# Kernel tuning notes

Hardware: AMD Instinct MI355X
Metric: run time of the kernel (lower is better)

## Reference

```python
import jax, jax.numpy as jnp
import numpy as np

EXPERT_NUM = 8
SEQ_LEN = 2048
FREQ_LEN = SEQ_LEN // 2 + 1
B, C = 32, 512


def setup_inputs() -> dict:
    key = jax.random.key(0)
    k1, k2, k3 = jax.random.split(key, 3)
    x = jax.random.normal(k1, (B, C, SEQ_LEN), dtype=jnp.float32)
    band_boundaries = jax.random.uniform(k2, (EXPERT_NUM - 1,), dtype=jnp.float32)
    gate_w = jax.random.normal(k3, (EXPERT_NUM, FREQ_LEN), dtype=jnp.float32) / np.sqrt(FREQ_LEN)
    gate_b = jnp.zeros((EXPERT_NUM,), dtype=jnp.float32)
    return {"x": x, "band_boundaries": band_boundaries, "gate_w": gate_w, "gate_b": gate_b}


def reference(x, band_boundaries, gate_w, gate_b):
    # x: [B, C, L].  Normalize across channels per (batch, time) position.
    xp = jnp.transpose(x, (0, 2, 1))                       # [B, L, C]
    x_mean = jnp.mean(xp, axis=2, keepdims=True)           # [B, L, 1]
    xc = xp - x_mean
    x_var = jnp.var(xc, axis=2, keepdims=True, ddof=1) + 1e-5  # unbiased, as torch.var
    xn = xc / jnp.sqrt(x_var)
    x_norm = jnp.transpose(xn, (0, 2, 1))                  # [B, C, L]

    freq_x = jnp.fft.rfft(x_norm, axis=-1)                 # [B, C, F] complex
    F = FREQ_LEN

    # Learnable band boundaries -> integer bin boundaries per expert.
    b = jnp.sort(jax.nn.sigmoid(band_boundaries))
    b = jnp.concatenate([jnp.zeros((1,), b.dtype), b, jnp.ones((1,), b.dtype)])
    idx = (b * F).astype(jnp.int32)
    idx = idx.at[-1].set(F)                                # [E+1]

    # Per-frequency-bin expert membership: [E, F] 0/1 mask.
    f = jnp.arange(F)
    member = ((f[None, :] >= idx[:-1, None]) & (f[None, :] < idx[1:, None])).astype(x.dtype)

    # Gating over mean spectral magnitude.
    gating_input = jnp.abs(freq_x).mean(axis=1)            # [B, F]
    gating_scores = jax.nn.softmax(gating_input @ gate_w.T + gate_b, axis=-1)  # [B, E]

    # Fused: per-bin gate weight = sum_e g[b,e] * member[e,f] (no E copies of freq_x).
    w = gating_scores @ member                             # [B, F]
    combined_freq = freq_x * w[:, None, :].astype(freq_x.dtype)

    combined = jnp.fft.irfft(combined_freq, n=SEQ_LEN, axis=-1)  # [B, C, L]

    # De-normalize.
    cp = jnp.transpose(combined, (0, 2, 1))                # [B, L, C]
    out = cp * jnp.sqrt(x_var) + x_mean
    return jnp.transpose(out, (0, 2, 1))                   # [B, C, L]
```

## Files before the change

### kernel.cpp

```cpp
#include <hip/hip_runtime.h>
#include <math.h>

#define NB 32
#define NC 512
#define NF 1025

#define WS_MEAN 0
#define WS_SSTD 65536
#define WS_RSTD 131072
#define WS_GACC 196608
#define WS_WGT  229408
#define WS_PART 262208
#define WS_END_SPLIT (262208 + 262144)
#define WS_SPEC WS_END_SPLIT
#define WS_SPEC_FLOATS (NB * NC * 2048)
#define WS_END_CACHE (WS_SPEC + WS_SPEC_FLOATS)

#define PIDX(a) ((a) + ((a) >> 4))

__device__ __forceinline__ void stage4(const float* __restrict__ sr,
                                       const float* __restrict__ si,
                                       float* __restrict__ dr,
                                       float* __restrict__ di,
                                       const int ls, const float w1c, const float w1s,
                                       const bool fwd) {
  const int t = threadIdx.x;
  const int s = 1 << ls;
  const int q = t & (s - 1);
  const int p = t >> ls;
  __syncthreads();
  const float ar = sr[PIDX(t)],       ai = si[PIDX(t)];
  const float br = sr[PIDX(t + 256)], bi = si[PIDX(t + 256)];
  const float cr = sr[PIDX(t + 512)], ci = si[PIDX(t + 512)];
  const float er = sr[PIDX(t + 768)], ei = si[PIDX(t + 768)];
  const float apcr = ar + cr, apci = ai + ci;
  const float amcr = ar - cr, amci = ai - ci;
  const float bpdr = br + er, bpdi = bi + ei;
  const float bmdr = br - er, bmdi = bi - ei;
  const float w2r = w1c * w1c - w1s * w1s, w2i = 2.0f * w1c * w1s;
  const float w3r = w2r * w1c - w2i * w1s, w3i = w2r * w1s + w2i * w1c;
  float u1r, u1i, u3r, u3i;
  if (fwd) {
    u1r = amcr + bmdi; u1i = amci - bmdr;
    u3r = amcr - bmdi; u3i = amci + bmdr;
  } else {
    u1r = amcr - bmdi; u1i = amci + bmdr;
    u3r = amcr + bmdi; u3i = amci - bmdr;
  }
  const float x0r = apcr + bpdr, x0i = apci + bpdi;
  const float v2r = apcr - bpdr, v2i = apci - bpdi;
  const float x1r = w1c * u1r - w1s * u1i, x1i = w1c * u1i + w1s * u1r;
  const float x2r = w2r * v2r - w2i * v2i, x2i = w2r * v2i + w2i * v2r;
  const float x3r = w3r * u3r - w3i * u3i, x3i = w3r * u3i + w3i * u3r;
  const int base = q + ((p << 2) << ls);
  dr[PIDX(base)] = x0r;             di[PIDX(base)] = x0i;
  dr[PIDX(base + s)] = x1r;         di[PIDX(base + s)] = x1i;
  dr[PIDX(base + 2 * s)] = x2r;     di[PIDX(base + 2 * s)] = x2i;
  dr[PIDX(base + 3 * s)] = x3r;     di[PIDX(base + 3 * s)] = x3i;
}

__device__ __forceinline__ void stage4_nt(const float* __restrict__ sr,
                                          const float* __restrict__ si,
                                          float* __restrict__ dr,
                                          float* __restrict__ di,
                                          const bool fwd) {
  const int t = threadIdx.x;
  __syncthreads();
  const float ar = sr[PIDX(t)],       ai = si[PIDX(t)];
  const float br = sr[PIDX(t + 256)], bi = si[PIDX(t + 256)];
  const float cr = sr[PIDX(t + 512)], ci = si[PIDX(t + 512)];
  const float er = sr[PIDX(t + 768)], ei = si[PIDX(t + 768)];
  const float apcr = ar + cr, apci = ai + ci;
  const float amcr = ar - cr, amci = ai - ci;
  const float bpdr = br + er, bpdi = bi + ei;
  const float bmdr = br - er, bmdi = bi - ei;
  float u1r, u1i, u3r, u3i;
  if (fwd) {
    u1r = amcr + bmdi; u1i = amci - bmdr;
    u3r = amcr - bmdi; u3i = amci + bmdr;
  } else {
    u1r = amcr - bmdi; u1i = amci + bmdr;
    u3r = amcr + bmdi; u3i = amci - bmdr;
  }
  dr[PIDX(t)] = apcr + bpdr;        di[PIDX(t)] = apci + bpdi;
  dr[PIDX(t + 256)] = u1r;          di[PIDX(t + 256)] = u1i;
  dr[PIDX(t + 512)] = apcr - bpdr;  di[PIDX(t + 512)] = apci - bpdi;
  dr[PIDX(t + 768)] = u3r;          di[PIDX(t + 768)] = u3i;
}

__device__ __forceinline__ void fft_twiddles(int t, float& c0, float& s0,
                                             float& c1, float& s1,
                                             float& c2, float& s2,
                                             float& c3, float& s3) {
  __sincosf(-0.00613592315f * (float)t, &s0, &c0);
  __sincosf(-0.02454369261f * (float)(t >> 2), &s1, &c1);
  __sincosf(-0.09817477042f * (float)(t >> 4), &s2, &c2);
  __sincosf(-0.39269908170f * (float)(t >> 6), &s3, &c3);
}

__device__ __forceinline__ void fft_fwd1024(float* Ar, float* Ai, float* Br, float* Bi,
                                            float c0, float s0, float c1, float s1,
                                            float c2, float s2, float c3, float s3) {
  stage4(Ar, Ai, Br, Bi, 0, c0, s0, true);
  stage4(Br, Bi, Ar, Ai, 2, c1, s1, true);
  stage4(Ar, Ai, Br, Bi, 4, c2, s2, true);
  stage4(Br, Bi, Ar, Ai, 6, c3, s3, true);
  stage4_nt(Ar, Ai, Br, Bi, true);
}
__device__ __forceinline__ void fft_inv1024(float* Ar, float* Ai, float* Br, float* Bi,
                                            float c0, float s0, float c1, float s1,
                                            float c2, float s2, float c3, float s3) {
  stage4(Br, Bi, Ar, Ai, 0, c0, -s0, false);
  stage4(Ar, Ai, Br, Bi, 2, c1, -s1, false);
  stage4(Br, Bi, Ar, Ai, 4, c2, -s2, false);
  stage4(Ar, Ai, Br, Bi, 6, c3, -s3, false);
  stage4_nt(Br, Bi, Ar, Ai, false);
}

__global__ __launch_bounds__(256) void kmoments(const float* __restrict__ x,
                                                float* __restrict__ ws) {
  const int b = blockIdx.x >> 3;
  const int l = ((blockIdx.x & 7) << 8) + threadIdx.x;
  const float* px = x + (size_t)b * (NC * 2048) + l;
  float sum = 0.f, sq = 0.f;
#pragma unroll 16
  for (int c = 0; c < NC; ++c) {
    float v = px[(size_t)c * 2048];
    sum += v;
    sq = fmaf(v, v, sq);
  }
  float mean = sum * (1.0f / 512.0f);
  float var = fmaf(-512.0f * mean, mean, sq) * (1.0f / 511.0f) + 1e-5f;
  float ss = sqrtf(var);
  int o = (b << 11) + l;
  ws[WS_MEAN + o] = mean;
  ws[WS_SSTD + o] = ss;
  ws[WS_RSTD + o] = 1.0f / ss;
}

__global__ __launch_bounds__(256) void kmoments_part(const float* __restrict__ x,
                                                     float* __restrict__ ws) {
  const int b = blockIdx.x >> 3;
  const int l = ((blockIdx.x & 7) << 8) + threadIdx.x;
  const int half = blockIdx.y;
  const float* px = x + (size_t)b * (NC * 2048) + (size_t)(half * 256) * 2048 + l;
  float sum = 0.f, sq = 0.f;
#pragma unroll 16
  for (int c = 0; c < 256; ++c) {
    float v = px[(size_t)c * 2048];
    sum += v;
    sq = fmaf(v, v, sq);
  }
  int o = (b << 11) + l;
  float2* part = (float2*)(ws + WS_PART) + (half << 16) + o;
  float2 pv; pv.x = sum; pv.y = sq;
  *part = pv;
}

__global__ __launch_bounds__(256) void kmoments_fin(float* __restrict__ ws) {
  const int o = blockIdx.x * 256 + threadIdx.x;
  const float2* part = (const float2*)(ws + WS_PART);
  float2 p0 = part[o];
  float2 p1 = part[(1 << 16) + o];
  float sum = p0.x + p1.x, sq = p0.y + p1.y;
  float mean = sum * (1.0f / 512.0f);
  float var = fmaf(-512.0f * mean, mean, sq) * (1.0f / 511.0f) + 1e-5f;
  float ss = sqrtf(var);
  ws[WS_MEAN + o] = mean;
  ws[WS_SSTD + o] = ss;
  ws[WS_RSTD + o] = 1.0f / ss;
}

__global__ __launch_bounds__(256) void kspec(const float* __restrict__ x,
                                             float* __restrict__ ws,
                                             float2* __restrict__ zout) {
  __shared__ float Ar[1088], Ai[1088], Br[1088], Bi[1088];
  const int tid = threadIdx.x;
  const int b = blockIdx.x >> 6;
  const int c0 = (blockIdx.x & 63) << 3;
  const float2* mean2 = (const float2*)(ws + WS_MEAN) + ((size_t)b << 10);
  const float2* rstd2 = (const float2*)(ws + WS_RSTD) + ((size_t)b << 10);
  float2 mv[4], rv[4];
#pragma unroll
  for (int j = 0; j < 4; ++j) {
    mv[j] = mean2[tid + (j << 8)];
    rv[j] = rstd2[tid + (j << 8)];
  }
  float w1s, w1c, w2s, w2c;
  __sincosf(-0.00306796158f * (float)tid, &w1s, &w1c);
  __sincosf(-0.00306796158f * (float)(tid + 256), &w2s, &w2c);
  float c0t, s0t, c1t, s1t, c2t, s2t, c3t, s3t;
  fft_twiddles(tid, c0t, s0t, c1t, s1t, c2t, s2t, c3t, s3t);
  float acc0 = 0.f, acc1 = 0.f, acc2 = 0.f, acc3 = 0.f, acc4 = 0.f;
  const float2* xrow = (const float2*)x + ((size_t)(b * NC + c0) << 10);
  float2 v[4];
#pragma unroll
  for (int j = 0; j < 4; ++j) v[j] = xrow[tid + (j << 8)];
  for (int r = 0; r < 8; ++r) {
#pragma unroll
    for (int j = 0; j < 4; ++j) {
      const int n = tid + (j << 8);
      Ar[PIDX(n)] = (v[j].x - mv[j].x) * rv[j].x;
      Ai[PIDX(n)] = (v[j].y - mv[j].y) * rv[j].y;
    }
    if (r < 7) {
      const float2* nx = xrow + ((size_t)(r + 1) << 10);
#pragma unroll
      for (int j = 0; j < 4; ++j) v[j] = nx[tid + (j << 8)];
    }
    fft_fwd1024(Ar, Ai, Br, Bi, c0t, s0t, c1t, s1t, c2t, s2t, c3t, s3t);
    __syncthreads();
    if (zout) {
      float2* zrow = zout + ((size_t)(b * NC + c0 + r) << 10);
#pragma unroll
      for (int j = 0; j < 4; ++j) {
        const int n = tid + (j << 8);
        float2 zv; zv.x = Br[PIDX(n)]; zv.y = Bi[PIDX(n)];
        zrow[n] = zv;
      }
    }
    if (tid == 0) {
      float zr = Br[PIDX(0)], zi = Bi[PIDX(0)];
      acc0 += fabsf(zr + zi);
      acc1 += fabsf(zr - zi);
      float mr = Br[PIDX(512)], mi = Bi[PIDX(512)];
      acc4 += sqrtf(mr * mr + mi * mi);
    } else {
      const int k = tid;
      float zkr = Br[PIDX(k)], zki = Bi[PIDX(k)];
      float zmr = Br[PIDX(1024 - k)], zmi = Bi[PIDX(1024 - k)];
      float Ar_ = 0.5f * (zkr + zmr), Ai_ = 0.5f * (zki - zmi);
      float Br_ = 0.5f * (zki + zmi), Bi_ = -0.5f * (zkr - zmr);
      float WBr = Br_ * w1c - Bi_ * w1s, WBi = Br_ * w1s + Bi_ * w1c;
      float Xr = Ar_ + WBr, Xi = Ai_ + WBi;
      float Yr = Ar_ - WBr, Yi = Ai_ - WBi;
      acc0 += sqrtf(Xr * Xr + Xi * Xi);
      acc1 += sqrtf(Yr * Yr + Yi * Yi);
    }
    {
      const int k = tid + 256;
      float zkr = Br[PIDX(k)], zki = Bi[PIDX(k)];
      float zmr = Br[PIDX(1024 - k)], zmi = Bi[PIDX(1024 - k)];
      float Ar_ = 0.5f * (zkr + zmr), Ai_ = 0.5f * (zki - zmi);
      float Br_ = 0.5f * (zki + zmi), Bi_ = -0.5f * (zkr - zmr);
      float WBr = Br_ * w2c - Bi_ * w2s, WBi = Br_ * w2s + Bi_ * w2c;
      float Xr = Ar_ + WBr, Xi = Ai_ + WBi;
      float Yr = Ar_ - WBr, Yi = Ai_ - WBi;
      acc2 += sqrtf(Xr * Xr + Xi * Xi);
      acc3 += sqrtf(Yr * Yr + Yi * Yi);
    }
  }
  float* g = ws + WS_GACC + b * NF;
  atomicAdd(g + tid, acc0);
  atomicAdd(g + 1024 - tid, acc1);
  atomicAdd(g + tid + 256, acc2);
  atomicAdd(g + 768 - tid, acc3);
  if (tid == 0) atomicAdd(g + 512, acc4);
}

__global__ __launch_bounds__(256) void kgate(float* __restrict__ ws,
                                             const float* __restrict__ gw,
                                             const float* __restrict__ gb,
                                             const float* __restrict__ bb) {
  const float* gacc = ws + WS_GACC;
  float* wgt = ws + WS_WGT;
  const int b = blockIdx.x;
  const int tid = threadIdx.x;
  __shared__ float red[256];
  __shared__ float sc[8];
  __shared__ int sidx[9];
  float acc[8];
#pragma unroll
  for (int e = 0; e < 8; ++e) acc[e] = 0.f;
  for (int f = tid; f < NF; f += 256) {
    float g = gacc[b * NF + f] * (1.0f / 512.0f);
#pragma unroll
    for (int e = 0; e < 8; ++e) acc[e] = fmaf(g, gw[e * NF + f], acc[e]);
  }
#pragma unroll
  for (int e = 0; e < 8; ++e) {
    __syncthreads();
    red[tid] = acc[e];
    __syncthreads();
    for (int s2 = 128; s2 > 0; s2 >>= 1) {
      if (tid < s2) red[tid] += red[tid + s2];
      __syncthreads();
    }
    if (tid == 0) sc[e] = red[0] + gb[e];
  }
  __syncthreads();
  if (tid == 0) {
    float mx = sc[0];
    for (int e = 1; e < 8; ++e) mx = fmaxf(mx, sc[e]);
    float sum = 0.f;
    float ex[8];
    for (int e = 0; e < 8; ++e) { ex[e] = expf(sc[e] - mx); sum += ex[e]; }
    for (int e = 0; e < 8; ++e) sc[e] = ex[e] / sum;
    float sv[7];
    for (int i2 = 0; i2 < 7; ++i2) sv[i2] = 1.0f / (1.0f + expf(-bb[i2]));
    for (int i2 = 1; i2 < 7; ++i2) {
      float key = sv[i2];
      int j2 = i2 - 1;
      while (j2 >= 0 && sv[j2] > key) { sv[j2 + 1] = sv[j2]; --j2; }
      sv[j2 + 1] = key;
    }
    sidx[0] = 0;
    for (int i2 = 0; i2 < 7; ++i2) sidx[i2 + 1] = (int)(sv[i2] * 1025.0f);
    sidx[8] = 1025;
  }
  __syncthreads();
  for (int f = tid; f < NF; f += 256) {
    float wv = 0.f;
#pragma unroll
    for (int e = 0; e < 8; ++e)
      if (f >= sidx[e] && f < sidx[e + 1]) wv += sc[e];
    wgt[b * NF + f] = wv;
  }
}

__device__ __forceinline__ void combine_pair(float* __restrict__ zr_, float* __restrict__ zi_,
                                             int k, float wc, float ws_, float wk, float wmk) {
  const int ik = PIDX(k), im = PIDX(1024 - k);
  float zkr = zr_[ik], zki = zi_[ik];
  float zmr = zr_[im], zmi = zi_[im];
  float Ar_ = 0.5f * (zkr + zmr), Ai_ = 0.5f * (zki - zmi);
  float Br2 = 0.5f * (zki + zmi), Bi2 = -0.5f * (zkr - zmr);
  float WBr = Br2 * wc - Bi2 * ws_, WBi = Br2 * ws_ + Bi2 * wc;
  float Xr = Ar_ + WBr, Xi = Ai_ + WBi;
  float Xcr = Ar_ - WBr, Xci = Ai_ - WBi;
  float XpR = wk * Xr, XpI = wk * Xi;
  float XcpR = wmk * Xcr, XcpI = wmk * Xci;
  float Apr = 0.5f * (XpR + XcpR), Api = 0.5f * (XpI + XcpI);
  float Er = 0.5f * (XpR - XcpR), Ei = 0.5f * (XpI - XcpI);
  float Bpr = Er * wc + Ei * ws_;
  float Bpi = Ei * wc - Er * ws_;
  zr_[ik] = Apr - Bpi;  zi_[ik] = Api + Bpr;
  zr_[im] = Apr + Bpi;  zi_[im] = Bpr - Api;
}

__global__ __launch_bounds__(256) void kapply(const float* __restrict__ x,
                                              float* __restrict__ out,
                                              const float* __restrict__ ws) {
  __shared__ float Ar[1088], Ai[1088], Br[1088], Bi[1088];
  const int tid = threadIdx.x;
  const int b = blockIdx.x >> 9;
  const float2* mean2 = (const float2*)(ws + WS_MEAN) + ((size_t)b << 10);
  const float2* sstd2 = (const float2*)(ws + WS_SSTD) + ((size_t)b << 10);
  const float2* rstd2 = (const float2*)(ws + WS_RSTD) + ((size_t)b << 10);
  const float2* x2 = (const float2*)x + ((size_t)blockIdx.x << 10);
  const float* wrow = ws + WS_WGT + b * NF;
  float wk1 = wrow[tid];
  float wm1 = wrow[1024 - tid];
  float wk2 = wrow[tid + 256];
  float wm2 = wrow[768 - tid];
  float wmid = wrow[512];
  float w1s, w1c, w2s, w2c;
  __sincosf(-0.00306796158f * (float)tid, &w1s, &w1c);
  __sincosf(-0.00306796158f * (float)(tid + 256), &w2s, &w2c);
  float c0t, s0t, c1t, s1t, c2t, s2t, c3t, s3t;
  fft_twiddles(tid, c0t, s0t, c1t, s1t, c2t, s2t, c3t, s3t);
  float2 mv[4], rv[4];
#pragma unroll
  for (int j = 0; j < 4; ++j) {
    mv[j] = mean2[tid + (j << 8)];
    rv[j] = rstd2[tid + (j << 8)];
  }
#pragma unroll
  for (int j = 0; j < 4; ++j) {
    const int n = tid + (j << 8);
    float2 v = x2[n];
    Ar[PIDX(n)] = (v.x - mv[j].x) * rv[j].x;
    Ai[PIDX(n)] = (v.y - mv[j].y) * rv[j].y;
  }
  fft_fwd1024(Ar, Ai, Br, Bi, c0t, s0t, c1t, s1t, c2t, s2t, c3t, s3t);
  __syncthreads();
  if (tid == 0) {
    float zr = Br[PIDX(0)], zi = Bi[PIDX(0)];
    float X0 = (zr + zi) * wk1;
    float XM = (zr - zi) * wm1;
    Br[PIDX(0)] = 0.5f * (X0 + XM);
    Bi[PIDX(0)] = 0.5f * (X0 - XM);
    Br[PIDX(512)] *= wmid;
    Bi[PIDX(512)] *= wmid;
  } else {
    combine_pair(Br, Bi, tid, w1c, w1s, wk1, wm1);
  }
  combine_pair(Br, Bi, tid + 256, w2c, w2s, wk2, wm2);
  fft_inv1024(Ar, Ai, Br, Bi, c0t, s0t, c1t, s1t, c2t, s2t, c3t, s3t);
  const float inv = 1.0f / 1024.0f;
  float2* out2 = (float2*)out + ((size_t)blockIdx.x << 10);
#pragma unroll
  for (int j = 0; j < 4; ++j) {
    const int n = tid + (j << 8);
    float2 ss = sstd2[n];
    float2 o;
    o.x = fmaf(Ar[PIDX(n)] * inv, ss.x, mv[j].x);
    o.y = fmaf(Ai[PIDX(n)] * inv, ss.y, mv[j].y);
    out2[n] = o;
  }
}

__global__ __launch_bounds__(256) void kapply_z(const float2* __restrict__ z,
                                                float* __restrict__ out,
                                                const float* __restrict__ ws) {
  __shared__ float Ar[1088], Ai[1088], Br[1088], Bi[1088];
  const int tid = threadIdx.x;
  const int b = blockIdx.x >> 9;
  const float2* mean2 = (const float2*)(ws + WS_MEAN) + ((size_t)b << 10);
  const float2* sstd2 = (const float2*)(ws + WS_SSTD) + ((size_t)b << 10);
  const float* wrow = ws + WS_WGT + b * NF;
  float wk1 = wrow[tid];
  float wm1 = wrow[1024 - tid];
  float wk2 = wrow[tid + 256];
  float wm2 = wrow[768 - tid];
  float wmid = wrow[512];
  float w1s, w1c, w2s, w2c;
  __sincosf(-0.00306796158f * (float)tid, &w1s, &w1c);
  __sincosf(-0.00306796158f * (float)(tid + 256), &w2s, &w2c);
  float c0t, s0t, c1t, s1t, c2t, s2t, c3t, s3t;
  fft_twiddles(tid, c0t, s0t, c1t, s1t, c2t, s2t, c3t, s3t);
  const float2* zrow = z + ((size_t)blockIdx.x << 10);
  float2 mv[4], ssv[4];
#pragma unroll
  for (int j = 0; j < 4; ++j) {
    mv[j] = mean2[tid + (j << 8)];
    ssv[j] = sstd2[tid + (j << 8)];
  }
#pragma unroll
  for (int j = 0; j < 4; ++j) {
    const int n = tid + (j << 8);
    float2 v = zrow[n];
    Br[PIDX(n)] = v.x;
    Bi[PIDX(n)] = v.y;
  }
  __syncthreads();
  if (tid == 0) {
    float zr = Br[PIDX(0)], zi = Bi[PIDX(0)];
    float X0 = (zr + zi) * wk1;
    float XM = (zr - zi) * wm1;
    Br[PIDX(0)] = 0.5f * (X0 + XM);
    Bi[PIDX(0)] = 0.5f * (X0 - XM);
    Br[PIDX(512)] *= wmid;
    Bi[PIDX(512)] *= wmid;
  } else {
    combine_pair(Br, Bi, tid, w1c, w1s, wk1, wm1);
  }
  combine_pair(Br, Bi, tid + 256, w2c, w2s, wk2, wm2);
  fft_inv1024(Ar, Ai, Br, Bi, c0t, s0t, c1t, s1t, c2t, s2t, c3t, s3t);
  const float inv = 1.0f / 1024.0f;
  float2* out2 = (float2*)out + ((size_t)blockIdx.x << 10);
#pragma unroll
  for (int j = 0; j < 4; ++j) {
    const int n = tid + (j << 8);
    float2 o;
    o.x = fmaf(Ar[PIDX(n)] * inv, ssv[j].x, mv[j].x);
    o.y = fmaf(Ai[PIDX(n)] * inv, ssv[j].y, mv[j].y);
    out2[n] = o;
  }
}

extern "C" void kernel_launch(void* const* d_in, const int* in_sizes, int n_in,
                              void* d_out, int out_size, void* d_ws, size_t ws_size,
                              hipStream_t stream) {
  const float* x = (const float*)d_in[0];
  const float* bb = (const float*)d_in[1];
  const float* gw = (const float*)d_in[2];
  const float* gb = (const float*)d_in[3];
  float* ws = (float*)d_ws;
  float* out = (float*)d_out;

  const bool split = ws_size >= (size_t)WS_END_SPLIT * sizeof(float);
  const bool cache = ws_size >= (size_t)WS_END_CACHE * sizeof(float);

  hipMemsetAsync((char*)d_ws + WS_GACC * sizeof(float), 0, (NB * NF) * sizeof(float), stream);
  if (split) {
    kmoments_part<<<dim3(NB * 8, 2), dim3(256), 0, stream>>>(x, ws);
    kmoments_fin<<<dim3(256), dim3(256), 0, stream>>>(ws);
  } else {
    kmoments<<<dim3(NB * 8), dim3(256), 0, stream>>>(x, ws);
  }
  kspec<<<dim3(NB * 64), dim3(256), 0, stream>>>(x, ws,
      cache ? (float2*)(ws + WS_SPEC) : nullptr);
  kgate<<<dim3(NB), dim3(256), 0, stream>>>(ws, gw, gb, bb);
  if (cache) {
    kapply_z<<<dim3(NB * NC), dim3(256), 0, stream>>>((const float2*)(ws + WS_SPEC), out, ws);
  } else {
    kapply<<<dim3(NB * NC), dim3(256), 0, stream>>>(x, out, ws);
  }
}
```

Measured before the change: 350.4 us.

## Keep first and last FFT stages in registers and replace gating atomics with partials

The first radix-4 FFT stage now reads its inputs directly from registers instead of staging them through shared memory. The final stage returns its results in registers, which feed the global writes and the output denormalisation directly, saving LDS round trips and one barrier per FFT. Gating magnitude sums are now written as per-block partials to an extra workspace region and reduced in kgate. This removes the atomics and the memset, but makes kgate read 64 rows per batch element.

```diff
diff --git a/kernel.cpp b/kernel.cpp
--- a/kernel.cpp
+++ b/kernel.cpp
@@ -15,6 +15,9 @@
 #define WS_SPEC WS_END_SPLIT
 #define WS_SPEC_FLOATS (NB * NC * 2048)
 #define WS_END_CACHE (WS_SPEC + WS_SPEC_FLOATS)
+#define WS_GPART WS_END_CACHE
+#define WS_GPART_FLOATS (NB * 64 * NF)
+#define WS_END_GPART (WS_GPART + WS_GPART_FLOATS)
 
 #define PIDX(a) ((a) + ((a) >> 4))
 
@@ -59,11 +62,42 @@
   dr[PIDX(base + 3 * s)] = x3r;     di[PIDX(base + 3 * s)] = x3i;
 }
 
-__device__ __forceinline__ void stage4_nt(const float* __restrict__ sr,
-                                          const float* __restrict__ si,
-                                          float* __restrict__ dr,
-                                          float* __restrict__ di,
-                                          const bool fwd) {
+__device__ __forceinline__ void stage0_reg(const float2 z0, const float2 z1,
+                                           const float2 z2, const float2 z3,
+                                           float* __restrict__ dr, float* __restrict__ di,
+                                           const float w1c, const float w1s,
+                                           const bool fwd) {
+  const int t = threadIdx.x;
+  const float apcr = z0.x + z2.x, apci = z0.y + z2.y;
+  const float amcr = z0.x - z2.x, amci = z0.y - z2.y;
+  const float bpdr = z1.x + z3.x, bpdi = z1.y + z3.y;
+  const float bmdr = z1.x - z3.x, bmdi = z1.y - z3.y;
+  const float w2r = w1c * w1c - w1s * w1s, w2i = 2.0f * w1c * w1s;
+  const float w3r = w2r * w1c - w2i * w1s, w3i = w2r * w1s + w2i * w1c;
+  float u1r, u1i, u3r, u3i;
+  if (fwd) {
+    u1r = amcr + bmdi; u1i = amci - bmdr;
+    u3r = amcr - bmdi; u3i = amci + bmdr;
+  } else {
+    u1r = amcr - bmdi; u1i = amci + bmdr;
+    u3r = amcr + bmdi; u3i = amci - bmdr;
+  }
+  const float x0r = apcr + bpdr, x0i = apci + bpdi;
+  const float v2r = apcr - bpdr, v2i = apci - bpdi;
+  const float x1r = w1c * u1r - w1s * u1i, x1i = w1c * u1i + w1s * u1r;
+  const float x2r = w2r * v2r - w2i * v2i, x2i = w2r * v2i + w2i * v2r;
+  const float x3r = w3r * u3r - w3i * u3i, x3i = w3r * u3i + w3i * u3r;
+  const int base = t << 2;
+  dr[PIDX(base)] = x0r;         di[PIDX(base)] = x0i;
+  dr[PIDX(base + 1)] = x1r;     di[PIDX(base + 1)] = x1i;
+  dr[PIDX(base + 2)] = x2r;     di[PIDX(base + 2)] = x2i;
+  dr[PIDX(base + 3)] = x3r;     di[PIDX(base + 3)] = x3i;
+}
+
+__device__ __forceinline__ void stage_nt_reg(const float* __restrict__ sr,
+                                             const float* __restrict__ si,
+                                             float2& o0, float2& o1, float2& o2, float2& o3,
+                                             const bool fwd) {
   const int t = threadIdx.x;
   __syncthreads();
   const float ar = sr[PIDX(t)],       ai = si[PIDX(t)];
@@ -82,10 +116,10 @@
     u1r = amcr - bmdi; u1i = amci + bmdr;
     u3r = amcr + bmdi; u3i = amci - bmdr;
   }
-  dr[PIDX(t)] = apcr + bpdr;        di[PIDX(t)] = apci + bpdi;
-  dr[PIDX(t + 256)] = u1r;          di[PIDX(t + 256)] = u1i;
-  dr[PIDX(t + 512)] = apcr - bpdr;  di[PIDX(t + 512)] = apci - bpdi;
-  dr[PIDX(t + 768)] = u3r;          di[PIDX(t + 768)] = u3i;
+  o0.x = apcr + bpdr;  o0.y = apci + bpdi;
+  o1.x = u1r;          o1.y = u1i;
+  o2.x = apcr - bpdr;  o2.y = apci - bpdi;
+  o3.x = u3r;          o3.y = u3i;
 }
 
 __device__ __forceinline__ void fft_twiddles(int t, float& c0, float& s0,
@@ -96,25 +130,6 @@
   __sincosf(-0.02454369261f * (float)(t >> 2), &s1, &c1);
   __sincosf(-0.09817477042f * (float)(t >> 4), &s2, &c2);
   __sincosf(-0.39269908170f * (float)(t >> 6), &s3, &c3);
-}
-
-__device__ __forceinline__ void fft_fwd1024(float* Ar, float* Ai, float* Br, float* Bi,
-                                            float c0, float s0, float c1, float s1,
-                                            float c2, float s2, float c3, float s3) {
-  stage4(Ar, Ai, Br, Bi, 0, c0, s0, true);
-  stage4(Br, Bi, Ar, Ai, 2, c1, s1, true);
-  stage4(Ar, Ai, Br, Bi, 4, c2, s2, true);
-  stage4(Br, Bi, Ar, Ai, 6, c3, s3, true);
-  stage4_nt(Ar, Ai, Br, Bi, true);
-}
-__device__ __forceinline__ void fft_inv1024(float* Ar, float* Ai, float* Br, float* Bi,
-                                            float c0, float s0, float c1, float s1,
-                                            float c2, float s2, float c3, float s3) {
-  stage4(Br, Bi, Ar, Ai, 0, c0, -s0, false);
-  stage4(Ar, Ai, Br, Bi, 2, c1, -s1, false);
-  stage4(Br, Bi, Ar, Ai, 4, c2, -s2, false);
-  stage4(Ar, Ai, Br, Bi, 6, c3, -s3, false);
-  stage4_nt(Br, Bi, Ar, Ai, false);
 }
 
 __global__ __launch_bounds__(256) void kmoments(const float* __restrict__ x,
@@ -173,7 +188,8 @@
 
 __global__ __launch_bounds__(256) void kspec(const float* __restrict__ x,
                                              float* __restrict__ ws,
-                                             float2* __restrict__ zout) {
+                                             float2* __restrict__ zout,
+                                             float* __restrict__ gpart) {
   __shared__ float Ar[1088], Ai[1088], Br[1088], Bi[1088];
   const int tid = threadIdx.x;
   const int b = blockIdx.x >> 6;
@@ -197,27 +213,35 @@
 #pragma unroll
   for (int j = 0; j < 4; ++j) v[j] = xrow[tid + (j << 8)];
   for (int r = 0; r < 8; ++r) {
+    float2 zz[4];
 #pragma unroll
     for (int j = 0; j < 4; ++j) {
-      const int n = tid + (j << 8);
-      Ar[PIDX(n)] = (v[j].x - mv[j].x) * rv[j].x;
-      Ai[PIDX(n)] = (v[j].y - mv[j].y) * rv[j].y;
+      zz[j].x = (v[j].x - mv[j].x) * rv[j].x;
+      zz[j].y = (v[j].y - mv[j].y) * rv[j].y;
     }
     if (r < 7) {
       const float2* nx = xrow + ((size_t)(r + 1) << 10);
 #pragma unroll
       for (int j = 0; j < 4; ++j) v[j] = nx[tid + (j << 8)];
     }
-    fft_fwd1024(Ar, Ai, Br, Bi, c0t, s0t, c1t, s1t, c2t, s2t, c3t, s3t);
+    __syncthreads();
+    stage0_reg(zz[0], zz[1], zz[2], zz[3], Br, Bi, c0t, s0t, true);
+    stage4(Br, Bi, Ar, Ai, 2, c1t, s1t, true);
+    stage4(Ar, Ai, Br, Bi, 4, c2t, s2t, true);
+    stage4(Br, Bi, Ar, Ai, 6, c3t, s3t, true);
+    float2 o0, o1, o2, o3;
+    stage_nt_reg(Ar, Ai, o0, o1, o2, o3, true);
+    Br[PIDX(tid)] = o0.x;        Bi[PIDX(tid)] = o0.y;
+    Br[PIDX(tid + 256)] = o1.x;  Bi[PIDX(tid + 256)] = o1.y;
+    Br[PIDX(tid + 512)] = o2.x;  Bi[PIDX(tid + 512)] = o2.y;
+    Br[PIDX(tid + 768)] = o3.x;  Bi[PIDX(tid + 768)] = o3.y;
     __syncthreads();
     if (zout) {
       float2* zrow = zout + ((size_t)(b * NC + c0 + r) << 10);
-#pragma unroll
-      for (int j = 0; j < 4; ++j) {
-        const int n = tid + (j << 8);
-        float2 zv; zv.x = Br[PIDX(n)]; zv.y = Bi[PIDX(n)];
-        zrow[n] = zv;
-      }
+      zrow[tid] = o0;
+      zrow[tid + 256] = o1;
+      zrow[tid + 512] = o2;
+      zrow[tid + 768] = o3;
     }
     if (tid == 0) {
       float zr = Br[PIDX(0)], zi = Bi[PIDX(0)];
@@ -250,18 +274,28 @@
       acc3 += sqrtf(Yr * Yr + Yi * Yi);
     }
   }
-  float* g = ws + WS_GACC + b * NF;
-  atomicAdd(g + tid, acc0);
-  atomicAdd(g + 1024 - tid, acc1);
-  atomicAdd(g + tid + 256, acc2);
-  atomicAdd(g + 768 - tid, acc3);
-  if (tid == 0) atomicAdd(g + 512, acc4);
+  if (gpart) {
+    float* prow = gpart + (size_t)blockIdx.x * NF;
+    prow[tid] = acc0;
+    prow[1024 - tid] = acc1;
+    prow[tid + 256] = acc2;
+    prow[768 - tid] = acc3;
+    if (tid == 0) prow[512] = acc4;
+  } else {
+    float* g = ws + WS_GACC + b * NF;
+    atomicAdd(g + tid, acc0);
+    atomicAdd(g + 1024 - tid, acc1);
+    atomicAdd(g + tid + 256, acc2);
+    atomicAdd(g + 768 - tid, acc3);
+    if (tid == 0) atomicAdd(g + 512, acc4);
+  }
 }
 
 __global__ __launch_bounds__(256) void kgate(float* __restrict__ ws,
                                              const float* __restrict__ gw,
                                              const float* __restrict__ gb,
-                                             const float* __restrict__ bb) {
+                                             const float* __restrict__ bb,
+                                             const float* __restrict__ gpart) {
   const float* gacc = ws + WS_GACC;
   float* wgt = ws + WS_WGT;
   const int b = blockIdx.x;
@@ -273,7 +307,16 @@
 #pragma unroll
   for (int e = 0; e < 8; ++e) acc[e] = 0.f;
   for (int f = tid; f < NF; f += 256) {
-    float g = gacc[b * NF + f] * (1.0f / 512.0f);
+    float g;
+    if (gpart) {
+      const float* gp = gpart + (size_t)b * 64 * NF + f;
+      g = 0.f;
+#pragma unroll 8
+      for (int j = 0; j < 64; ++j) g += gp[j * NF];
+    } else {
+      g = gacc[b * NF + f];
+    }
+    g *= (1.0f / 512.0f);
 #pragma unroll
     for (int e = 0; e < 8; ++e) acc[e] = fmaf(g, gw[e * NF + f], acc[e]);
   }
@@ -359,20 +402,30 @@
   __sincosf(-0.00306796158f * (float)(tid + 256), &w2s, &w2c);
   float c0t, s0t, c1t, s1t, c2t, s2t, c3t, s3t;
   fft_twiddles(tid, c0t, s0t, c1t, s1t, c2t, s2t, c3t, s3t);
-  float2 mv[4], rv[4];
+  float2 mv[4], rv[4], ssv[4];
 #pragma unroll
   for (int j = 0; j < 4; ++j) {
     mv[j] = mean2[tid + (j << 8)];
     rv[j] = rstd2[tid + (j << 8)];
-  }
+    ssv[j] = sstd2[tid + (j << 8)];
+  }
+  float2 zz[4];
 #pragma unroll
   for (int j = 0; j < 4; ++j) {
-    const int n = tid + (j << 8);
-    float2 v = x2[n];
-    Ar[PIDX(n)] = (v.x - mv[j].x) * rv[j].x;
-    Ai[PIDX(n)] = (v.y - mv[j].y) * rv[j].y;
-  }
-  fft_fwd1024(Ar, Ai, Br, Bi, c0t, s0t, c1t, s1t, c2t, s2t, c3t, s3t);
+    float2 v = x2[tid + (j << 8)];
+    zz[j].x = (v.x - mv[j].x) * rv[j].x;
+    zz[j].y = (v.y - mv[j].y) * rv[j].y;
+  }
+  stage0_reg(zz[0], zz[1], zz[2], zz[3], Br, Bi, c0t, s0t, true);
+  stage4(Br, Bi, Ar, Ai, 2, c1t, s1t, true);
+  stage4(Ar, Ai, Br, Bi, 4, c2t, s2t, true);
+  stage4(Br, Bi, Ar, Ai, 6, c3t, s3t, true);
+  float2 f0, f1, f2, f3;
+  stage_nt_reg(Ar, Ai, f0, f1, f2, f3, true);
+  Br[PIDX(tid)] = f0.x;        Bi[PIDX(tid)] = f0.y;
+  Br[PIDX(tid + 256)] = f1.x;  Bi[PIDX(tid + 256)] = f1.y;
+  Br[PIDX(tid + 512)] = f2.x;  Bi[PIDX(tid + 512)] = f2.y;
+  Br[PIDX(tid + 768)] = f3.x;  Bi[PIDX(tid + 768)] = f3.y;
   __syncthreads();
   if (tid == 0) {
     float zr = Br[PIDX(0)], zi = Bi[PIDX(0)];
@@ -386,18 +439,27 @@
     combine_pair(Br, Bi, tid, w1c, w1s, wk1, wm1);
   }
   combine_pair(Br, Bi, tid + 256, w2c, w2s, wk2, wm2);
-  fft_inv1024(Ar, Ai, Br, Bi, c0t, s0t, c1t, s1t, c2t, s2t, c3t, s3t);
+  stage4(Br, Bi, Ar, Ai, 0, c0t, -s0t, false);
+  stage4(Ar, Ai, Br, Bi, 2, c1t, -s1t, false);
+  stage4(Br, Bi, Ar, Ai, 4, c2t, -s2t, false);
+  stage4(Ar, Ai, Br, Bi, 6, c3t, -s3t, false);
+  float2 o0, o1, o2, o3;
+  stage_nt_reg(Br, Bi, o0, o1, o2, o3, false);
   const float inv = 1.0f / 1024.0f;
   float2* out2 = (float2*)out + ((size_t)blockIdx.x << 10);
-#pragma unroll
-  for (int j = 0; j < 4; ++j) {
-    const int n = tid + (j << 8);
-    float2 ss = sstd2[n];
-    float2 o;
-    o.x = fmaf(Ar[PIDX(n)] * inv, ss.x, mv[j].x);
-    o.y = fmaf(Ai[PIDX(n)] * inv, ss.y, mv[j].y);
-    out2[n] = o;
-  }
+  float2 oo;
+  oo.x = fmaf(o0.x * inv, ssv[0].x, mv[0].x);
+  oo.y = fmaf(o0.y * inv, ssv[0].y, mv[0].y);
+  out2[tid] = oo;
+  oo.x = fmaf(o1.x * inv, ssv[1].x, mv[1].x);
+  oo.y = fmaf(o1.y * inv, ssv[1].y, mv[1].y);
+  out2[tid + 256] = oo;
+  oo.x = fmaf(o2.x * inv, ssv[2].x, mv[2].x);
+  oo.y = fmaf(o2.y * inv, ssv[2].y, mv[2].y);
+  out2[tid + 512] = oo;
+  oo.x = fmaf(o3.x * inv, ssv[3].x, mv[3].x);
+  oo.y = fmaf(o3.y * inv, ssv[3].y, mv[3].y);
+  out2[tid + 768] = oo;
 }
 
 __global__ __launch_bounds__(256) void kapply_z(const float2* __restrict__ z,
@@ -446,17 +508,27 @@
     combine_pair(Br, Bi, tid, w1c, w1s, wk1, wm1);
   }
   combine_pair(Br, Bi, tid + 256, w2c, w2s, wk2, wm2);
-  fft_inv1024(Ar, Ai, Br, Bi, c0t, s0t, c1t, s1t, c2t, s2t, c3t, s3t);
+  stage4(Br, Bi, Ar, Ai, 0, c0t, -s0t, false);
+  stage4(Ar, Ai, Br, Bi, 2, c1t, -s1t, false);
+  stage4(Br, Bi, Ar, Ai, 4, c2t, -s2t, false);
+  stage4(Ar, Ai, Br, Bi, 6, c3t, -s3t, false);
+  float2 o0, o1, o2, o3;
+  stage_nt_reg(Br, Bi, o0, o1, o2, o3, false);
   const float inv = 1.0f / 1024.0f;
   float2* out2 = (float2*)out + ((size_t)blockIdx.x << 10);
-#pragma unroll
-  for (int j = 0; j < 4; ++j) {
-    const int n = tid + (j << 8);
-    float2 o;
-    o.x = fmaf(Ar[PIDX(n)] * inv, ssv[j].x, mv[j].x);
-    o.y = fmaf(Ai[PIDX(n)] * inv, ssv[j].y, mv[j].y);
-    out2[n] = o;
-  }
+  float2 oo;
+  oo.x = fmaf(o0.x * inv, ssv[0].x, mv[0].x);
+  oo.y = fmaf(o0.y * inv, ssv[0].y, mv[0].y);
+  out2[tid] = oo;
+  oo.x = fmaf(o1.x * inv, ssv[1].x, mv[1].x);
+  oo.y = fmaf(o1.y * inv, ssv[1].y, mv[1].y);
+  out2[tid + 256] = oo;
+  oo.x = fmaf(o2.x * inv, ssv[2].x, mv[2].x);
+  oo.y = fmaf(o2.y * inv, ssv[2].y, mv[2].y);
+  out2[tid + 512] = oo;
+  oo.x = fmaf(o3.x * inv, ssv[3].x, mv[3].x);
+  oo.y = fmaf(o3.y * inv, ssv[3].y, mv[3].y);
+  out2[tid + 768] = oo;
 }
 
 extern "C" void kernel_launch(void* const* d_in, const int* in_sizes, int n_in,
@@ -471,8 +543,11 @@
 
   const bool split = ws_size >= (size_t)WS_END_SPLIT * sizeof(float);
   const bool cache = ws_size >= (size_t)WS_END_CACHE * sizeof(float);
-
-  hipMemsetAsync((char*)d_ws + WS_GACC * sizeof(float), 0, (NB * NF) * sizeof(float), stream);
+  const bool part = ws_size >= (size_t)WS_END_GPART * sizeof(float);
+
+  if (!part) {
+    hipMemsetAsync((char*)d_ws + WS_GACC * sizeof(float), 0, (NB * NF) * sizeof(float), stream);
+  }
   if (split) {
     kmoments_part<<<dim3(NB * 8, 2), dim3(256), 0, stream>>>(x, ws);
     kmoments_fin<<<dim3(256), dim3(256), 0, stream>>>(ws);
@@ -480,8 +555,10 @@
     kmoments<<<dim3(NB * 8), dim3(256), 0, stream>>>(x, ws);
   }
   kspec<<<dim3(NB * 64), dim3(256), 0, stream>>>(x, ws,
-      cache ? (float2*)(ws + WS_SPEC) : nullptr);
-  kgate<<<dim3(NB), dim3(256), 0, stream>>>(ws, gw, gb, bb);
+      cache ? (float2*)(ws + WS_SPEC) : nullptr,
+      part ? (ws + WS_GPART) : nullptr);
+  kgate<<<dim3(NB), dim3(256), 0, stream>>>(ws, gw, gb, bb,
+      part ? (ws + WS_GPART) : nullptr);
   if (cache) {
     kapply_z<<<dim3(NB * NC), dim3(256), 0, stream>>>((const float2*)(ws + WS_SPEC), out, ws);
   } else {
```

New measurement: 352.1 us. Within noise of the previous version (+0.5%).
